# Optimization experiments

Hardware: AMD Instinct MI355X
Metric: run time of the kernel (lower is better)

The kernel has to match this reference:

```python
import jax, jax.numpy as jnp
import numpy as np

N_NODES = 100000
N_EDGES = 1600000
IN_SIZE = 128
HIDDEN = 128
OUT_SIZE = 64


def setup_inputs() -> dict:
    key = jax.random.key(0)
    k = jax.random.split(key, 8)
    feat = jax.random.normal(k[0], (N_NODES, IN_SIZE), dtype=jnp.float32)
    src = jax.random.randint(k[1], (N_EDGES,), 0, N_NODES, dtype=jnp.int32)
    dst = jax.random.randint(k[2], (N_EDGES,), 0, N_NODES, dtype=jnp.int32)
    # fc_neigh weights for the two SAGEConv layers (stored as [in, out])
    W1 = jax.random.normal(k[3], (IN_SIZE, HIDDEN), dtype=jnp.float32) / np.sqrt(IN_SIZE)
    b1 = jnp.zeros((HIDDEN,), dtype=jnp.float32)
    W2 = jax.random.normal(k[4], (HIDDEN, OUT_SIZE), dtype=jnp.float32) / np.sqrt(HIDDEN)
    b2 = jnp.zeros((OUT_SIZE,), dtype=jnp.float32)
    return {"feat": feat, "W1": W1, "b1": b1, "W2": W2, "b2": b2,
            "src": src, "dst": dst}


def _sage_gcn(h, src, dst, W, b):
    # DGL SAGEConv with aggregator_type='gcn':
    #   neigh = segment_sum over incoming edges of src features
    #   h_neigh = (neigh + h_self) / (in_degree + 1)
    #   out = h_neigh @ W + b   (fc_self is not used for 'gcn')
    neigh = jax.ops.segment_sum(h[src], dst, num_segments=N_NODES)  # [N, d]
    deg = jax.ops.segment_sum(jnp.ones((src.shape[0],), dtype=h.dtype), dst,
                              num_segments=N_NODES)                 # [N]
    h_neigh = (neigh + h) / (deg + 1.0)[:, None]
    return h_neigh @ W + b


def reference(feat, W1, b1, W2, b2, src, dst):
    # dropout(p=0.0) is identity; activation between layers only
    h = _sage_gcn(feat, src, dst, W1, b1)
    h = jax.nn.relu(h)
    h = _sage_gcn(h, src, dst, W2, b2)
    return h
```

## Files before the change

kernel.cpp:

```cpp
#include <hip/hip_runtime.h>

#define NNODES 100000
#define NEDGES 1600000
#define BSHIFT 7
#define NB 782
#define CAP 2560
#define EBLOCKS 391
#define GEMM_BLOCKS 1563

typedef _Float16 f16;
typedef _Float16 v4h __attribute__((ext_vector_type(4)));
typedef _Float16 v8h __attribute__((ext_vector_type(8)));
typedef float v4f __attribute__((ext_vector_type(4)));

__global__ __launch_bounds__(256) void init_k(int* __restrict__ bcur,
                                              const float* __restrict__ W1,
                                              f16* __restrict__ W1t,
                                              const float* __restrict__ W2,
                                              f16* __restrict__ W2t) {
    int t = blockIdx.x * 256 + threadIdx.x;
    if (t < NB) bcur[t] = t * CAP;
    int u = t - 1024;
    if (u >= 0) {
        if (u < 128 * 128) {
            int k = u >> 7, n = u & 127;
            W1t[n * 128 + k] = (f16)W1[k * 128 + n];
        } else if (u < 128 * 128 + 128 * 64) {
            int v = u - 128 * 128;
            int k = v >> 6, n = v & 63;
            W2t[n * 128 + k] = (f16)W2[k * 64 + n];
        }
    }
}

__global__ __launch_bounds__(256) void scatter_gemm1(
    const int* __restrict__ src, const int* __restrict__ dst,
    int* __restrict__ bcur, int* __restrict__ ebuf,
    const float* __restrict__ feat, const f16* __restrict__ W1t,
    f16* __restrict__ z1) {
    constexpr int PITCH = 136;
    __shared__ __align__(16) char smem[128 * PITCH * 2];
    int tid = threadIdx.x;

    if (blockIdx.x < EBLOCKS) {
        int* h = (int*)smem;
        int* base_s = ((int*)smem) + 1024;
        for (int i = tid; i < NB; i += 256) h[i] = 0;
        __syncthreads();
        int base = blockIdx.x * 4096;
        int d[16], sv[16];
        for (int k = 0; k < 16; k++) {
            int e = base + k * 256 + tid;
            if (e < NEDGES) {
                d[k] = dst[e];
                sv[k] = src[e];
                atomicAdd(&h[d[k] >> BSHIFT], 1);
            } else {
                d[k] = -1;
            }
        }
        __syncthreads();
        for (int i = tid; i < NB; i += 256) {
            int c = h[i];
            if (c) base_s[i] = atomicAdd(&bcur[i], c);
            h[i] = 0;
        }
        __syncthreads();
        for (int k = 0; k < 16; k++) {
            if (d[k] >= 0) {
                int b = d[k] >> BSHIFT;
                int slot = atomicAdd(&h[b], 1);
                ebuf[base_s[b] + slot] = sv[k] | ((d[k] & 127) << 24);
            }
        }
        return;
    }

    f16* wlds = (f16*)smem;
    for (int c = tid; c < 128 * 16; c += 256) {
        int n = c >> 4;
        int kc = c & 15;
        *(v8h*)&wlds[n * PITCH + kc * 8] = *(const v8h*)&W1t[n * 128 + kc * 8];
    }
    __syncthreads();

    int wave = tid >> 6, lane = tid & 63, quad = lane >> 4, l16 = lane & 15;
    int m0 = (blockIdx.x - EBLOCKS) * 64 + wave * 16;
    if (m0 >= NNODES) return;

    v8h a[4];
    const float* arow = feat + (long)(m0 + l16) * 128 + quad * 8;
#pragma unroll
    for (int kb = 0; kb < 4; kb++) {
        float4 f0 = *(const float4*)(arow + kb * 32);
        float4 f1 = *(const float4*)(arow + kb * 32 + 4);
        v8h t = {(f16)f0.x, (f16)f0.y, (f16)f0.z, (f16)f0.w,
                 (f16)f1.x, (f16)f1.y, (f16)f1.z, (f16)f1.w};
        a[kb] = t;
    }

#pragma unroll
    for (int nt = 0; nt < 8; nt++) {
        v4f acc = {0.f, 0.f, 0.f, 0.f};
        const f16* brow = &wlds[(nt * 16 + l16) * PITCH + quad * 8];
#pragma unroll
        for (int kb = 0; kb < 4; kb++) {
            v8h b = *(const v8h*)(brow + kb * 32);
            acc = __builtin_amdgcn_mfma_f32_16x16x32_f16(a[kb], b, acc, 0, 0, 0);
        }
        int n = nt * 16 + l16;
#pragma unroll
        for (int r = 0; r < 4; r++)
            z1[(long)(m0 + quad * 4 + r) * 128 + n] = (f16)acc[r];
    }
}

__global__ __launch_bounds__(256) void fill_bucket(const int* __restrict__ ebuf,
                                                   const int* __restrict__ bcur,
                                                   int* __restrict__ begs,
                                                   int* __restrict__ ends,
                                                   int* __restrict__ csr) {
    __shared__ int lc[128];
    __shared__ int ls[256];
    int b = blockIdx.x;
    int tid = threadIdx.x;
    if (tid < 128) lc[tid] = 0;
    __syncthreads();
    int ebeg = b * CAP;
    int eend = bcur[b];
    for (int e = ebeg + tid; e < eend; e += 256)
        atomicAdd(&lc[((unsigned)ebuf[e]) >> 24], 1);
    __syncthreads();
    int cnt = (tid < 128) ? lc[tid] : 0;
    ls[tid] = cnt;
    __syncthreads();
    for (int off = 1; off < 256; off <<= 1) {
        int t = (tid >= off) ? ls[tid - off] : 0;
        __syncthreads();
        ls[tid] += t;
        __syncthreads();
    }
    int excl = ls[tid] - cnt;
    int node = (b << BSHIFT) + tid;
    if (tid < 128 && node < NNODES) {
        begs[node] = ebeg + excl;
        ends[node] = ebeg + excl + cnt;
    }
    if (tid < 128) { ls[tid] = excl; lc[tid] = 0; }
    __syncthreads();
    for (int e = ebeg + tid; e < eend; e += 256) {
        int p = ebuf[e];
        int dloc = ((unsigned)p) >> 24;
        int slot = atomicAdd(&lc[dloc], 1);
        csr[ebeg + ls[dloc] + slot] = p & 0xFFFFFF;
    }
}

__global__ __launch_bounds__(1024, 8) void gather128_gemm2(
    const f16* __restrict__ z,
    const int* __restrict__ begs, const int* __restrict__ ends,
    const int* __restrict__ csr,
    const float* __restrict__ b1,
    const f16* __restrict__ W2t,
    f16* __restrict__ z2)
{
    constexpr int PITCH = 136;
    __shared__ f16 w2lds[64 * PITCH];
    __shared__ f16 atile[16 * PITCH];
    int tid = threadIdx.x;

    {
        int n = tid >> 4, kc = tid & 15;
        *(v8h*)&w2lds[n * PITCH + kc * 8] = *(const v8h*)&W2t[n * 128 + kc * 8];
    }

    int wavei = tid >> 6;
    int lane = tid & 63;
    int sub = lane >> 4;
    int c = lane & 15;
    int node = blockIdx.x * 16 + wavei;

    int beg = begs[node];
    int end = ends[node];

    const char* zb = (const char*)z;
    unsigned coff = (unsigned)c << 4;

    v8h sv = {0, 0, 0, 0, 0, 0, 0, 0};
    if (sub == 0) sv = *(const v8h*)(zb + ((unsigned)node << 8) + coff);

    float af[8];
#pragma unroll
    for (int j = 0; j < 8; j++) af[j] = 0.f;

    for (int e = beg; e < end; e += 32) {
        v8h u0 = {0,0,0,0,0,0,0,0}, u1 = {0,0,0,0,0,0,0,0};
        v8h u2 = {0,0,0,0,0,0,0,0}, u3 = {0,0,0,0,0,0,0,0};
        v8h u4 = {0,0,0,0,0,0,0,0}, u5 = {0,0,0,0,0,0,0,0};
        v8h u6 = {0,0,0,0,0,0,0,0}, u7 = {0,0,0,0,0,0,0,0};
        int i;
        i = e + sub;      if (i < end) u0 = *(const v8h*)(zb + (((unsigned)csr[i]) << 8) + coff);
        i = e + 4 + sub;  if (i < end) u1 = *(const v8h*)(zb + (((unsigned)csr[i]) << 8) + coff);
        i = e + 8 + sub;  if (i < end) u2 = *(const v8h*)(zb + (((unsigned)csr[i]) << 8) + coff);
        i = e + 12 + sub; if (i < end) u3 = *(const v8h*)(zb + (((unsigned)csr[i]) << 8) + coff);
        i = e + 16 + sub; if (i < end) u4 = *(const v8h*)(zb + (((unsigned)csr[i]) << 8) + coff);
        i = e + 20 + sub; if (i < end) u5 = *(const v8h*)(zb + (((unsigned)csr[i]) << 8) + coff);
        i = e + 24 + sub; if (i < end) u6 = *(const v8h*)(zb + (((unsigned)csr[i]) << 8) + coff);
        i = e + 28 + sub; if (i < end) u7 = *(const v8h*)(zb + (((unsigned)csr[i]) << 8) + coff);
        asm volatile("" : "+v"(u0), "+v"(u1), "+v"(u2), "+v"(u3),
                          "+v"(u4), "+v"(u5), "+v"(u6), "+v"(u7));
        v8h s01 = u0 + u1, s23 = u2 + u3, s45 = u4 + u5, s67 = u6 + u7;
        v8h s03 = s01 + s23, s47 = s45 + s67;
        v8h s = s03 + s47;
#pragma unroll
        for (int j = 0; j < 8; j++) af[j] += (float)s[j];
    }
#pragma unroll
    for (int j = 0; j < 8; j++) af[j] += (float)sv[j];

#pragma unroll
    for (int j = 0; j < 8; j++) {
        af[j] += __shfl_xor(af[j], 16);
        af[j] += __shfl_xor(af[j], 32);
    }

    if (sub == 0) {
        float inv = 1.0f / (float)(end - beg + 1);
        float4 bb0 = ((const float4*)b1)[c * 2];
        float4 bb1 = ((const float4*)b1)[c * 2 + 1];
        v8h o = {(f16)fmaxf(af[0] * inv + bb0.x, 0.f),
                 (f16)fmaxf(af[1] * inv + bb0.y, 0.f),
                 (f16)fmaxf(af[2] * inv + bb0.z, 0.f),
                 (f16)fmaxf(af[3] * inv + bb0.w, 0.f),
                 (f16)fmaxf(af[4] * inv + bb1.x, 0.f),
                 (f16)fmaxf(af[5] * inv + bb1.y, 0.f),
                 (f16)fmaxf(af[6] * inv + bb1.z, 0.f),
                 (f16)fmaxf(af[7] * inv + bb1.w, 0.f)};
        *(v8h*)&atile[wavei * PITCH + c * 8] = o;
    }
    __syncthreads();

    if (wavei < 4) {
        int quad = lane >> 4, l16 = lane & 15;
        const f16* arow = &atile[l16 * PITCH + quad * 8];
        const f16* brow = &w2lds[(wavei * 16 + l16) * PITCH + quad * 8];
        v4f acc = {0.f, 0.f, 0.f, 0.f};
#pragma unroll
        for (int kb = 0; kb < 4; kb++) {
            v8h av = *(const v8h*)(arow + kb * 32);
            v8h bv = *(const v8h*)(brow + kb * 32);
            acc = __builtin_amdgcn_mfma_f32_16x16x32_f16(av, bv, acc, 0, 0, 0);
        }
        int n = wavei * 16 + l16;
        int m0 = blockIdx.x * 16;
#pragma unroll
        for (int r = 0; r < 4; r++)
            z2[(long)(m0 + quad * 4 + r) * 64 + n] = (f16)acc[r];
    }
}

__global__ __launch_bounds__(256, 8) void gather64(
    const f16* __restrict__ z, const int* __restrict__ begs,
    const int* __restrict__ ends, const int* __restrict__ csr,
    const float* __restrict__ bias, float4* __restrict__ out) {
    int node = (int)(((long)blockIdx.x * blockDim.x + threadIdx.x) >> 6);
    if (node >= NNODES) return;
    int lane = threadIdx.x & 63;
    int sub = lane >> 3;
    int c = lane & 7;

    int beg = begs[node];
    int end = ends[node];

    const char* zb = (const char*)z;
    unsigned coff = (unsigned)c << 4;

    v8h sv = {0, 0, 0, 0, 0, 0, 0, 0};
    if (sub == 0) sv = *(const v8h*)(zb + ((unsigned)node << 7) + coff);

    float af[8];
#pragma unroll
    for (int j = 0; j < 8; j++) af[j] = 0.f;

    for (int e = beg; e < end; e += 64) {
        v8h u0 = {0,0,0,0,0,0,0,0}, u1 = {0,0,0,0,0,0,0,0};
        v8h u2 = {0,0,0,0,0,0,0,0}, u3 = {0,0,0,0,0,0,0,0};
        v8h u4 = {0,0,0,0,0,0,0,0}, u5 = {0,0,0,0,0,0,0,0};
        v8h u6 = {0,0,0,0,0,0,0,0}, u7 = {0,0,0,0,0,0,0,0};
        int i;
        i = e + sub;      if (i < end) u0 = *(const v8h*)(zb + (((unsigned)csr[i]) << 7) + coff);
        i = e + 8 + sub;  if (i < end) u1 = *(const v8h*)(zb + (((unsigned)csr[i]) << 7) + coff);
        i = e + 16 + sub; if (i < end) u2 = *(const v8h*)(zb + (((unsigned)csr[i]) << 7) + coff);
        i = e + 24 + sub; if (i < end) u3 = *(const v8h*)(zb + (((unsigned)csr[i]) << 7) + coff);
        i = e + 32 + sub; if (i < end) u4 = *(const v8h*)(zb + (((unsigned)csr[i]) << 7) + coff);
        i = e + 40 + sub; if (i < end) u5 = *(const v8h*)(zb + (((unsigned)csr[i]) << 7) + coff);
        i = e + 48 + sub; if (i < end) u6 = *(const v8h*)(zb + (((unsigned)csr[i]) << 7) + coff);
        i = e + 56 + sub; if (i < end) u7 = *(const v8h*)(zb + (((unsigned)csr[i]) << 7) + coff);
        asm volatile("" : "+v"(u0), "+v"(u1), "+v"(u2), "+v"(u3),
                          "+v"(u4), "+v"(u5), "+v"(u6), "+v"(u7));
        v8h s01 = u0 + u1, s23 = u2 + u3, s45 = u4 + u5, s67 = u6 + u7;
        v8h s03 = s01 + s23, s47 = s45 + s67;
        v8h s = s03 + s47;
#pragma unroll
        for (int j = 0; j < 8; j++) af[j] += (float)s[j];
    }
#pragma unroll
    for (int j = 0; j < 8; j++) af[j] += (float)sv[j];

#pragma unroll
    for (int j = 0; j < 8; j++) {
        af[j] += __shfl_xor(af[j], 8);
        af[j] += __shfl_xor(af[j], 16);
        af[j] += __shfl_xor(af[j], 32);
    }

    if (sub == 0) {
        float inv = 1.0f / (float)(end - beg + 1);
        float4 b0 = ((const float4*)bias)[c * 2];
        float4 b1v = ((const float4*)bias)[c * 2 + 1];
        out[(long)node * 16 + c * 2] =
            make_float4(af[0] * inv + b0.x, af[1] * inv + b0.y,
                        af[2] * inv + b0.z, af[3] * inv + b0.w);
        out[(long)node * 16 + c * 2 + 1] =
            make_float4(af[4] * inv + b1v.x, af[5] * inv + b1v.y,
                        af[6] * inv + b1v.z, af[7] * inv + b1v.w);
    }
}

extern "C" void kernel_launch(void* const* d_in, const int* in_sizes, int n_in,
                              void* d_out, int out_size, void* d_ws, size_t ws_size,
                              hipStream_t stream) {
    const float* feat = (const float*)d_in[0];
    const float* W1   = (const float*)d_in[1];
    const float* b1   = (const float*)d_in[2];
    const float* W2   = (const float*)d_in[3];
    const float* b2   = (const float*)d_in[4];
    const int*   src  = (const int*)d_in[5];
    const int*   dst  = (const int*)d_in[6];
    float* out = (float*)d_out;

    char* ws = (char*)d_ws;
    int* bcur = (int*)(ws + 0x0000000);
    int* begs = (int*)(ws + 0x0001000);
    int* ends = (int*)(ws + 0x0063000);
    int* csr  = (int*)(ws + 0x00C5000);
    int* ebuf = (int*)(ws + 0x0870000);
    f16* z1   = (f16*)(ws + 0x1100000);
    f16* z2   = (f16*)(ws + 0x2A00000);
    f16* W1t  = (f16*)(ws + 0x3700000);
    f16* W2t  = (f16*)(ws + 0x3710000);

    init_k<<<100, 256, 0, stream>>>(bcur, W1, W1t, W2, W2t);

    scatter_gemm1<<<EBLOCKS + GEMM_BLOCKS, 256, 0, stream>>>(src, dst, bcur, ebuf,
                                                             feat, W1t, z1);

    fill_bucket<<<NB, 256, 0, stream>>>(ebuf, bcur, begs, ends, csr);

    gather128_gemm2<<<NNODES / 16, 1024, 0, stream>>>(z1, begs, ends,
                                                      csr, b1, W2t, z2);

    gather64<<<(NNODES * 64 + 255) / 256, 256, 0, stream>>>(z2, begs,
                                                            ends, csr, b2,
                                                            (float4*)out);
}
```

Baseline: 255.1 us.

## Map one node per lane-group instead of one node per wave in gathers

Both gather kernels now give each node a 16-lane (layer 1) or 8-lane (layer 2) group instead of a full wave, so several nodes share a wave. This removes the cross-lane shuffle reductions. Each group walks its edges sequentially, 8 at a time, under a wave-wide __any loop. The fused GEMM2 block now handles 64 nodes and uses all 16 waves for MFMA tiles rather than 4. The trade-off is divergence: nodes of different degree share a wave, so the loop runs until the slowest node finishes, and each lane issues more dependent loads.

```diff
diff --git a/kernel.cpp b/kernel.cpp
--- a/kernel.cpp
+++ b/kernel.cpp
@@ -166,7 +166,7 @@
 {
     constexpr int PITCH = 136;
     __shared__ f16 w2lds[64 * PITCH];
-    __shared__ f16 atile[16 * PITCH];
+    __shared__ f16 atile[64 * PITCH];
     int tid = threadIdx.x;
 
     {
@@ -178,53 +178,48 @@
     int lane = tid & 63;
     int sub = lane >> 4;
     int c = lane & 15;
-    int node = blockIdx.x * 16 + wavei;
-
-    int beg = begs[node];
-    int end = ends[node];
+    int lnode = wavei * 4 + sub;
+    int node = blockIdx.x * 64 + lnode;
+
+    int beg = 0, end = 0;
+    if (node < NNODES) { beg = begs[node]; end = ends[node]; }
 
     const char* zb = (const char*)z;
     unsigned coff = (unsigned)c << 4;
 
-    v8h sv = {0, 0, 0, 0, 0, 0, 0, 0};
-    if (sub == 0) sv = *(const v8h*)(zb + ((unsigned)node << 8) + coff);
-
     float af[8];
 #pragma unroll
     for (int j = 0; j < 8; j++) af[j] = 0.f;
 
-    for (int e = beg; e < end; e += 32) {
+    if (node < NNODES) {
+        v8h sv = *(const v8h*)(zb + ((unsigned)node << 8) + coff);
+#pragma unroll
+        for (int j = 0; j < 8; j++) af[j] = (float)sv[j];
+    }
+
+    int e = beg;
+    while (__any(e < end)) {
         v8h u0 = {0,0,0,0,0,0,0,0}, u1 = {0,0,0,0,0,0,0,0};
         v8h u2 = {0,0,0,0,0,0,0,0}, u3 = {0,0,0,0,0,0,0,0};
         v8h u4 = {0,0,0,0,0,0,0,0}, u5 = {0,0,0,0,0,0,0,0};
         v8h u6 = {0,0,0,0,0,0,0,0}, u7 = {0,0,0,0,0,0,0,0};
-        int i;
-        i = e + sub;      if (i < end) u0 = *(const v8h*)(zb + (((unsigned)csr[i]) << 8) + coff);
-        i = e + 4 + sub;  if (i < end) u1 = *(const v8h*)(zb + (((unsigned)csr[i]) << 8) + coff);
-        i = e + 8 + sub;  if (i < end) u2 = *(const v8h*)(zb + (((unsigned)csr[i]) << 8) + coff);
-        i = e + 12 + sub; if (i < end) u3 = *(const v8h*)(zb + (((unsigned)csr[i]) << 8) + coff);
-        i = e + 16 + sub; if (i < end) u4 = *(const v8h*)(zb + (((unsigned)csr[i]) << 8) + coff);
-        i = e + 20 + sub; if (i < end) u5 = *(const v8h*)(zb + (((unsigned)csr[i]) << 8) + coff);
-        i = e + 24 + sub; if (i < end) u6 = *(const v8h*)(zb + (((unsigned)csr[i]) << 8) + coff);
-        i = e + 28 + sub; if (i < end) u7 = *(const v8h*)(zb + (((unsigned)csr[i]) << 8) + coff);
-        asm volatile("" : "+v"(u0), "+v"(u1), "+v"(u2), "+v"(u3),
-                          "+v"(u4), "+v"(u5), "+v"(u6), "+v"(u7));
+        if (e     < end) u0 = *(const v8h*)(zb + (((unsigned)csr[e    ]) << 8) + coff);
+        if (e + 1 < end) u1 = *(const v8h*)(zb + (((unsigned)csr[e + 1]) << 8) + coff);
+        if (e + 2 < end) u2 = *(const v8h*)(zb + (((unsigned)csr[e + 2]) << 8) + coff);
+        if (e + 3 < end) u3 = *(const v8h*)(zb + (((unsigned)csr[e + 3]) << 8) + coff);
+        if (e + 4 < end) u4 = *(const v8h*)(zb + (((unsigned)csr[e + 4]) << 8) + coff);
+        if (e + 5 < end) u5 = *(const v8h*)(zb + (((unsigned)csr[e + 5]) << 8) + coff);
+        if (e + 6 < end) u6 = *(const v8h*)(zb + (((unsigned)csr[e + 6]) << 8) + coff);
+        if (e + 7 < end) u7 = *(const v8h*)(zb + (((unsigned)csr[e + 7]) << 8) + coff);
         v8h s01 = u0 + u1, s23 = u2 + u3, s45 = u4 + u5, s67 = u6 + u7;
         v8h s03 = s01 + s23, s47 = s45 + s67;
         v8h s = s03 + s47;
 #pragma unroll
         for (int j = 0; j < 8; j++) af[j] += (float)s[j];
-    }
-#pragma unroll
-    for (int j = 0; j < 8; j++) af[j] += (float)sv[j];
-
-#pragma unroll
-    for (int j = 0; j < 8; j++) {
-        af[j] += __shfl_xor(af[j], 16);
-        af[j] += __shfl_xor(af[j], 32);
-    }
-
-    if (sub == 0) {
+        e += 8;
+    }
+
+    {
         float inv = 1.0f / (float)(end - beg + 1);
         float4 bb0 = ((const float4*)b1)[c * 2];
         float4 bb1 = ((const float4*)b1)[c * 2 + 1];
@@ -236,14 +231,15 @@
                  (f16)fmaxf(af[5] * inv + bb1.y, 0.f),
                  (f16)fmaxf(af[6] * inv + bb1.z, 0.f),
                  (f16)fmaxf(af[7] * inv + bb1.w, 0.f)};
-        *(v8h*)&atile[wavei * PITCH + c * 8] = o;
-    }
-    __syncthreads();
-
-    if (wavei < 4) {
+        *(v8h*)&atile[lnode * PITCH + c * 8] = o;
+    }
+    __syncthreads();
+
+    {
+        int wr = wavei >> 2, wc = wavei & 3;
         int quad = lane >> 4, l16 = lane & 15;
-        const f16* arow = &atile[l16 * PITCH + quad * 8];
-        const f16* brow = &w2lds[(wavei * 16 + l16) * PITCH + quad * 8];
+        const f16* arow = &atile[(wr * 16 + l16) * PITCH + quad * 8];
+        const f16* brow = &w2lds[(wc * 16 + l16) * PITCH + quad * 8];
         v4f acc = {0.f, 0.f, 0.f, 0.f};
 #pragma unroll
         for (int kb = 0; kb < 4; kb++) {
@@ -251,11 +247,13 @@
             v8h bv = *(const v8h*)(brow + kb * 32);
             acc = __builtin_amdgcn_mfma_f32_16x16x32_f16(av, bv, acc, 0, 0, 0);
         }
-        int n = wavei * 16 + l16;
-        int m0 = blockIdx.x * 16;
-#pragma unroll
-        for (int r = 0; r < 4; r++)
-            z2[(long)(m0 + quad * 4 + r) * 64 + n] = (f16)acc[r];
+        int n = wc * 16 + l16;
+        int m0 = blockIdx.x * 64 + wr * 16;
+#pragma unroll
+        for (int r = 0; r < 4; r++) {
+            int row = m0 + quad * 4 + r;
+            if (row < NNODES) z2[(long)row * 64 + n] = (f16)acc[r];
+        }
     }
 }
 
@@ -263,11 +261,10 @@
     const f16* __restrict__ z, const int* __restrict__ begs,
     const int* __restrict__ ends, const int* __restrict__ csr,
     const float* __restrict__ bias, float4* __restrict__ out) {
-    int node = (int)(((long)blockIdx.x * blockDim.x + threadIdx.x) >> 6);
-    if (node >= NNODES) return;
-    int lane = threadIdx.x & 63;
-    int sub = lane >> 3;
+    int tid = threadIdx.x;
+    int lane = tid & 63;
     int c = lane & 7;
+    int node = blockIdx.x * 32 + (tid >> 3);
 
     int beg = begs[node];
     int end = ends[node];
@@ -275,46 +272,36 @@
     const char* zb = (const char*)z;
     unsigned coff = (unsigned)c << 4;
 
-    v8h sv = {0, 0, 0, 0, 0, 0, 0, 0};
-    if (sub == 0) sv = *(const v8h*)(zb + ((unsigned)node << 7) + coff);
-
     float af[8];
-#pragma unroll
-    for (int j = 0; j < 8; j++) af[j] = 0.f;
-
-    for (int e = beg; e < end; e += 64) {
+    {
+        v8h sv = *(const v8h*)(zb + ((unsigned)node << 7) + coff);
+#pragma unroll
+        for (int j = 0; j < 8; j++) af[j] = (float)sv[j];
+    }
+
+    int e = beg;
+    while (__any(e < end)) {
         v8h u0 = {0,0,0,0,0,0,0,0}, u1 = {0,0,0,0,0,0,0,0};
         v8h u2 = {0,0,0,0,0,0,0,0}, u3 = {0,0,0,0,0,0,0,0};
         v8h u4 = {0,0,0,0,0,0,0,0}, u5 = {0,0,0,0,0,0,0,0};
         v8h u6 = {0,0,0,0,0,0,0,0}, u7 = {0,0,0,0,0,0,0,0};
-        int i;
-        i = e + sub;      if (i < end) u0 = *(const v8h*)(zb + (((unsigned)csr[i]) << 7) + coff);
-        i = e + 8 + sub;  if (i < end) u1 = *(const v8h*)(zb + (((unsigned)csr[i]) << 7) + coff);
-        i = e + 16 + sub; if (i < end) u2 = *(const v8h*)(zb + (((unsigned)csr[i]) << 7) + coff);
-        i = e + 24 + sub; if (i < end) u3 = *(const v8h*)(zb + (((unsigned)csr[i]) << 7) + coff);
-        i = e + 32 + sub; if (i < end) u4 = *(const v8h*)(zb + (((unsigned)csr[i]) << 7) + coff);
-        i = e + 40 + sub; if (i < end) u5 = *(const v8h*)(zb + (((unsigned)csr[i]) << 7) + coff);
-        i = e + 48 + sub; if (i < end) u6 = *(const v8h*)(zb + (((unsigned)csr[i]) << 7) + coff);
-        i = e + 56 + sub; if (i < end) u7 = *(const v8h*)(zb + (((unsigned)csr[i]) << 7) + coff);
-        asm volatile("" : "+v"(u0), "+v"(u1), "+v"(u2), "+v"(u3),
-                          "+v"(u4), "+v"(u5), "+v"(u6), "+v"(u7));
+        if (e     < end) u0 = *(const v8h*)(zb + (((unsigned)csr[e    ]) << 7) + coff);
+        if (e + 1 < end) u1 = *(const v8h*)(zb + (((unsigned)csr[e + 1]) << 7) + coff);
+        if (e + 2 < end) u2 = *(const v8h*)(zb + (((unsigned)csr[e + 2]) << 7) + coff);
+        if (e + 3 < end) u3 = *(const v8h*)(zb + (((unsigned)csr[e + 3]) << 7) + coff);
+        if (e + 4 < end) u4 = *(const v8h*)(zb + (((unsigned)csr[e + 4]) << 7) + coff);
+        if (e + 5 < end) u5 = *(const v8h*)(zb + (((unsigned)csr[e + 5]) << 7) + coff);
+        if (e + 6 < end) u6 = *(const v8h*)(zb + (((unsigned)csr[e + 6]) << 7) + coff);
+        if (e + 7 < end) u7 = *(const v8h*)(zb + (((unsigned)csr[e + 7]) << 7) + coff);
         v8h s01 = u0 + u1, s23 = u2 + u3, s45 = u4 + u5, s67 = u6 + u7;
         v8h s03 = s01 + s23, s47 = s45 + s67;
         v8h s = s03 + s47;
 #pragma unroll
         for (int j = 0; j < 8; j++) af[j] += (float)s[j];
-    }
-#pragma unroll
-    for (int j = 0; j < 8; j++) af[j] += (float)sv[j];
-
-#pragma unroll
-    for (int j = 0; j < 8; j++) {
-        af[j] += __shfl_xor(af[j], 8);
-        af[j] += __shfl_xor(af[j], 16);
-        af[j] += __shfl_xor(af[j], 32);
-    }
-
-    if (sub == 0) {
+        e += 8;
+    }
+
+    {
         float inv = 1.0f / (float)(end - beg + 1);
         float4 b0 = ((const float4*)bias)[c * 2];
         float4 b1v = ((const float4*)bias)[c * 2 + 1];
@@ -357,10 +344,7 @@
 
     fill_bucket<<<NB, 256, 0, stream>>>(ebuf, bcur, begs, ends, csr);
 
-    gather128_gemm2<<<NNODES / 16, 1024, 0, stream>>>(z1, begs, ends,
-                                                      csr, b1, W2t, z2);
-
-    gather64<<<(NNODES * 64 + 255) / 256, 256, 0, stream>>>(z2, begs,
-                                                            ends, csr, b2,
-                                                            (float4*)out);
-}
+    gather128_gemm2<<<1563, 1024, 0, stream>>>(z1, begs, ends, csr, b1, W2t, z2);
+
+    gather64<<<3125, 256, 0, stream>>>(z2, begs, ends, csr, b2, (float4*)out);
+}
```

After: 247.9 us. 1.03x faster.
